# Kernel tuning notes

Hardware: AMD Instinct MI355X
Metric: run time of the kernel (lower is better)

Reference implementation:

```python
import jax, jax.numpy as jnp
import numpy as np

B, T, D_MODEL, HEAD_DIM = 4, 4096, 1024, 2


def setup_inputs() -> dict:
    key = jax.random.key(0)
    kx, kq, kk, kv = jax.random.split(key, 4)
    x = jax.random.normal(kx, (B, T, D_MODEL), dtype=jnp.float32)
    # nn.Linear weights: (out_features, in_features), applied as x @ W.T
    s_qk = 1.0 / np.sqrt(D_MODEL)
    W_Q = jax.random.uniform(kq, (HEAD_DIM, D_MODEL), minval=-s_qk, maxval=s_qk, dtype=jnp.float32)
    W_K = jax.random.uniform(kk, (HEAD_DIM, D_MODEL), minval=-s_qk, maxval=s_qk, dtype=jnp.float32)
    W_V = jax.random.uniform(kv, (D_MODEL, D_MODEL), minval=-s_qk, maxval=s_qk, dtype=jnp.float32)
    # strict upper-triangular True = masked (future positions)
    causal_mask = jnp.triu(jnp.ones((T, T), dtype=bool), k=1)[None, :, :]
    return {"x": x, "W_Q": W_Q, "W_K": W_K, "W_V": W_V, "causal_mask": causal_mask}


def reference(x, W_Q, W_K, W_V, causal_mask):
    # x: (B, T, d_model)
    Q = jnp.einsum('btd,hd->bth', x, W_Q)   # (B, T, head_dim)
    K = jnp.einsum('bsd,hd->bsh', x, W_K)   # (B, S, head_dim)
    V = jnp.einsum('bsd,ed->bse', x, W_V)   # (B, S, d_model)
    scores = jnp.einsum('bth,bsh->bts', Q, K)              # (B, T, S)
    scores = jnp.where(causal_mask, -jnp.inf, scores)
    max_idx = jnp.argmax(scores, axis=-1)                  # (B, T)
    # one-hot scatter + bmm in the original == hard gather of V rows
    out = jnp.take_along_axis(V, max_idx[..., None], axis=1)  # (B, T, d_model)
    return out
```

## Files before the change

### kernel.cpp

```cpp
#include <hip/hip_runtime.h>
#include <math.h>

#define TT 4096
#define DM 1024
#define BB 4
#define BT (BB * TT)
#define SENTINEL 0x7fffffff


__device__ __forceinline__ float dot4(const float4 a, const float4 b) {
    return a.x * b.x + a.y * b.y + a.z * b.z + a.w * b.w;
}

__global__ __launch_bounds__(256) void qk_kernel(const float* __restrict__ x,
                                                 const float* __restrict__ wq,
                                                 const float* __restrict__ wk,
                                                 float* __restrict__ Q,
                                                 float* __restrict__ K,
                                                 int* __restrict__ rep,
                                                 int* __restrict__ cnt) {
    __shared__ float4 wqs0[256], wqs1[256], wks0[256], wks1[256];
    const int tid = threadIdx.x;
    const int row0 = blockIdx.x * 4;

    wqs0[tid] = ((const float4*)(wq))[tid];
    wqs1[tid] = ((const float4*)(wq + DM))[tid];
    wks0[tid] = ((const float4*)(wk))[tid];
    wks1[tid] = ((const float4*)(wk + DM))[tid];

    if (tid < 4) rep[row0 + tid] = SENTINEL;
    if (blockIdx.x == 0 && tid == 4) cnt[0] = 0;
    __syncthreads();

    const int wave = tid >> 6, lane = tid & 63;
    const int row = row0 + wave;
    const float4* xr = (const float4*)(x + (size_t)row * DM);

    float s0 = 0.f, s1 = 0.f, s2 = 0.f, s3 = 0.f;
    #pragma unroll
    for (int j = 0; j < 4; ++j) {
        const float4 xv = xr[j * 64 + lane];
        s0 += dot4(xv, wqs0[j * 64 + lane]);
        s1 += dot4(xv, wqs1[j * 64 + lane]);
        s2 += dot4(xv, wks0[j * 64 + lane]);
        s3 += dot4(xv, wks1[j * 64 + lane]);
    }
    #pragma unroll
    for (int off = 32; off > 0; off >>= 1) {
        s0 += __shfl_down(s0, off);
        s1 += __shfl_down(s1, off);
        s2 += __shfl_down(s2, off);
        s3 += __shfl_down(s3, off);
    }
    if (lane == 0) {
        ((float2*)Q)[row] = make_float2(s0, s1);
        ((float2*)K)[row] = make_float2(s2, s3);
    }
}

__global__ __launch_bounds__(256) void argmax_kernel(const float* __restrict__ Q,
                                                     const float* __restrict__ K,
                                                     int* __restrict__ idx,
                                                     int* __restrict__ rep,
                                                     int* __restrict__ list,
                                                     int* __restrict__ cnt) {
    __shared__ float2 ks[TT];
    const int b  = blockIdx.x >> 10;
    const int tg = blockIdx.x & 1023;
    const int tid = threadIdx.x;
    const int nfill = tg * 4 + 4;

    const float2* kb = (const float2*)(K + (size_t)b * TT * 2);
    for (int i = tid; i < nfill; i += 256) ks[i] = kb[i];
    __syncthreads();

    const int wave = tid >> 6, lane = tid & 63;
    const int t = tg * 4 + wave;
    const float2 q = ((const float2*)Q)[b * TT + t];

    float best = -INFINITY;
    int bi = 0x7fffffff;
    int s = lane;
    while (s + 192 <= t) {
        const float2 k0 = ks[s];
        const float2 k1 = ks[s + 64];
        const float2 k2 = ks[s + 128];
        const float2 k3 = ks[s + 192];
        const float c0 = q.x * k0.x + q.y * k0.y;
        const float c1 = q.x * k1.x + q.y * k1.y;
        const float c2 = q.x * k2.x + q.y * k2.y;
        const float c3 = q.x * k3.x + q.y * k3.y;
        if (c0 > best) { best = c0; bi = s; }
        if (c1 > best) { best = c1; bi = s + 64; }
        if (c2 > best) { best = c2; bi = s + 128; }
        if (c3 > best) { best = c3; bi = s + 192; }
        s += 256;
    }
    while (s <= t) {
        const float2 kv = ks[s];
        const float sc = q.x * kv.x + q.y * kv.y;
        if (sc > best) { best = sc; bi = s; }
        s += 64;
    }
    #pragma unroll
    for (int off = 32; off > 0; off >>= 1) {
        const float ov = __shfl_down(best, off);
        const int   oi = __shfl_down(bi, off);
        if (ov > best || (ov == best && oi < bi)) { best = ov; bi = oi; }
    }
    if (lane == 0) {
        idx[b * TT + t] = bi;
        const int old = atomicMin(&rep[b * TT + bi], t);
        if (old == SENTINEL) {
            const int p = atomicAdd(cnt, 1);
            list[p] = b * TT + bi;
        }
    }
}

__global__ __launch_bounds__(256) void vrow_kernel(const float* __restrict__ x,
                                                   const float* __restrict__ wv,
                                                   const int* __restrict__ rep,
                                                   const int* __restrict__ list,
                                                   const int* __restrict__ cnt,
                                                   float* __restrict__ out) {
    const int tid = threadIdx.x, wave = tid >> 6, lane = tid & 63;
    const int slice = blockIdx.x >> 3;
    const int usub  = blockIdx.x & 7;
    const int e = slice * 4 + wave;

    const float4* wrow = (const float4*)(wv + (size_t)e * DM);
    const float4 w0 = wrow[lane];
    const float4 w1 = wrow[lane + 64];
    const float4 w2 = wrow[lane + 128];
    const float4 w3 = wrow[lane + 192];

    const int n = cnt[0];
    for (int li = usub; li < n; li += 8) {
        const int bs = list[li];
        const int b  = bs >> 12;
        const int r  = rep[bs];
        const float4* xr = (const float4*)(x + (size_t)bs * DM);
        const float4 x0 = xr[lane];
        const float4 x1 = xr[lane + 64];
        const float4 x2 = xr[lane + 128];
        const float4 x3 = xr[lane + 192];

        float sum = dot4(w0, x0) + dot4(w1, x1) + dot4(w2, x2) + dot4(w3, x3);
        #pragma unroll
        for (int off = 32; off > 0; off >>= 1) sum += __shfl_down(sum, off);
        if (lane == 0) out[((size_t)(b * TT + r)) * DM + e] = sum;
    }
}

__global__ __launch_bounds__(256) void gather_kernel(const int* __restrict__ idx,
                                                     const int* __restrict__ rep,
                                                     float* __restrict__ out) {
    const int bt = blockIdx.x;
    const int b = bt >> 12, t = bt & (TT - 1);
    const int s = idx[bt];
    const int r = rep[b * TT + s];
    if (r == t) return;
    const float4* src = (const float4*)(out + ((size_t)(b * TT + r)) * DM);
    float4* dst = (float4*)(out + (size_t)bt * DM);
    dst[threadIdx.x] = src[threadIdx.x];
}

extern "C" void kernel_launch(void* const* d_in, const int* in_sizes, int n_in,
                              void* d_out, int out_size, void* d_ws, size_t ws_size,
                              hipStream_t stream) {
    const float* x  = (const float*)d_in[0];
    const float* wq = (const float*)d_in[1];
    const float* wk = (const float*)d_in[2];
    const float* wv = (const float*)d_in[3];
    float* out = (float*)d_out;

    char* ws = (char*)d_ws;
    float* Q    = (float*)(ws);
    float* K    = (float*)(ws + 131072);
    int*   idx  = (int*)  (ws + 262144);
    int*   rep  = (int*)  (ws + 327680);
    int*   list = (int*)  (ws + 393216);
    int*   cnt  = (int*)  (ws + 458752);

    qk_kernel<<<BT / 4, 256, 0, stream>>>(x, wq, wk, Q, K, rep, cnt);
    argmax_kernel<<<4096, 256, 0, stream>>>(Q, K, idx, rep, list, cnt);
    vrow_kernel<<<2048, 256, 0, stream>>>(x, wv, rep, list, cnt, out);
    gather_kernel<<<BT, 256, 0, stream>>>(idx, rep, out);
}
```

Baseline: 228.5 us.

## Vectorize argmax key loads and compute four V outputs per wave

The argmax scan now reads two keys per float4 LDS load and handles four keys per iteration with fewer load instructions. The V-row kernel gives each wave four W_V rows held in registers, so each loaded x row feeds four dot products. It writes the four results as one float4 and launches half as many blocks with a 16-way stride over the unique-row list. This trades more registers per thread and fewer blocks for less redundant x traffic and fewer shuffle reductions per output.

```diff
diff --git a/kernel.cpp b/kernel.cpp
--- a/kernel.cpp
+++ b/kernel.cpp
@@ -77,30 +77,33 @@
     const int wave = tid >> 6, lane = tid & 63;
     const int t = tg * 4 + wave;
     const float2 q = ((const float2*)Q)[b * TT + t];
+    const float4* kp = (const float4*)ks;
 
     float best = -INFINITY;
     int bi = 0x7fffffff;
-    int s = lane;
-    while (s + 192 <= t) {
-        const float2 k0 = ks[s];
-        const float2 k1 = ks[s + 64];
-        const float2 k2 = ks[s + 128];
-        const float2 k3 = ks[s + 192];
-        const float c0 = q.x * k0.x + q.y * k0.y;
-        const float c1 = q.x * k1.x + q.y * k1.y;
-        const float c2 = q.x * k2.x + q.y * k2.y;
-        const float c3 = q.x * k3.x + q.y * k3.y;
-        if (c0 > best) { best = c0; bi = s; }
-        if (c1 > best) { best = c1; bi = s + 64; }
-        if (c2 > best) { best = c2; bi = s + 128; }
-        if (c3 > best) { best = c3; bi = s + 192; }
-        s += 256;
-    }
-    while (s <= t) {
-        const float2 kv = ks[s];
-        const float sc = q.x * kv.x + q.y * kv.y;
-        if (sc > best) { best = sc; bi = s; }
-        s += 64;
+    int p = lane;
+    while (2 * (p + 64) + 1 <= t) {
+        const float4 a = kp[p];
+        const float4 c = kp[p + 64];
+        const float c0 = q.x * a.x + q.y * a.y;
+        const float c1 = q.x * a.z + q.y * a.w;
+        const float c2 = q.x * c.x + q.y * c.y;
+        const float c3 = q.x * c.z + q.y * c.w;
+        if (c0 > best) { best = c0; bi = 2 * p; }
+        if (c1 > best) { best = c1; bi = 2 * p + 1; }
+        if (c2 > best) { best = c2; bi = 2 * (p + 64); }
+        if (c3 > best) { best = c3; bi = 2 * (p + 64) + 1; }
+        p += 128;
+    }
+    while (2 * p <= t) {
+        const float4 a = kp[p];
+        const float c0 = q.x * a.x + q.y * a.y;
+        if (c0 > best) { best = c0; bi = 2 * p; }
+        if (2 * p + 1 <= t) {
+            const float c1 = q.x * a.z + q.y * a.w;
+            if (c1 > best) { best = c1; bi = 2 * p + 1; }
+        }
+        p += 64;
     }
     #pragma unroll
     for (int off = 32; off > 0; off >>= 1) {
@@ -112,8 +115,8 @@
         idx[b * TT + t] = bi;
         const int old = atomicMin(&rep[b * TT + bi], t);
         if (old == SENTINEL) {
-            const int p = atomicAdd(cnt, 1);
-            list[p] = b * TT + bi;
+            const int pp = atomicAdd(cnt, 1);
+            list[pp] = b * TT + bi;
         }
     }
 }
@@ -125,31 +128,45 @@
                                                    const int* __restrict__ cnt,
                                                    float* __restrict__ out) {
     const int tid = threadIdx.x, wave = tid >> 6, lane = tid & 63;
-    const int slice = blockIdx.x >> 3;
-    const int usub  = blockIdx.x & 7;
-    const int e = slice * 4 + wave;
-
-    const float4* wrow = (const float4*)(wv + (size_t)e * DM);
-    const float4 w0 = wrow[lane];
-    const float4 w1 = wrow[lane + 64];
-    const float4 w2 = wrow[lane + 128];
-    const float4 w3 = wrow[lane + 192];
+    const int slice = blockIdx.x >> 4;
+    const int usub  = blockIdx.x & 15;
+    const int e0 = slice * 16 + wave * 4;
+
+    float4 w[4][4];
+    #pragma unroll
+    for (int r = 0; r < 4; ++r) {
+        const float4* wr = (const float4*)(wv + (size_t)(e0 + r) * DM);
+        #pragma unroll
+        for (int j = 0; j < 4; ++j) w[r][j] = wr[j * 64 + lane];
+    }
 
     const int n = cnt[0];
-    for (int li = usub; li < n; li += 8) {
+    for (int li = usub; li < n; li += 16) {
         const int bs = list[li];
         const int b  = bs >> 12;
         const int r  = rep[bs];
         const float4* xr = (const float4*)(x + (size_t)bs * DM);
-        const float4 x0 = xr[lane];
-        const float4 x1 = xr[lane + 64];
-        const float4 x2 = xr[lane + 128];
-        const float4 x3 = xr[lane + 192];
-
-        float sum = dot4(w0, x0) + dot4(w1, x1) + dot4(w2, x2) + dot4(w3, x3);
-        #pragma unroll
-        for (int off = 32; off > 0; off >>= 1) sum += __shfl_down(sum, off);
-        if (lane == 0) out[((size_t)(b * TT + r)) * DM + e] = sum;
+        float4 xv[4];
+        #pragma unroll
+        for (int j = 0; j < 4; ++j) xv[j] = xr[j * 64 + lane];
+
+        float s0 = 0.f, s1 = 0.f, s2 = 0.f, s3 = 0.f;
+        #pragma unroll
+        for (int j = 0; j < 4; ++j) {
+            s0 += dot4(w[0][j], xv[j]);
+            s1 += dot4(w[1][j], xv[j]);
+            s2 += dot4(w[2][j], xv[j]);
+            s3 += dot4(w[3][j], xv[j]);
+        }
+        #pragma unroll
+        for (int off = 32; off > 0; off >>= 1) {
+            s0 += __shfl_down(s0, off);
+            s1 += __shfl_down(s1, off);
+            s2 += __shfl_down(s2, off);
+            s3 += __shfl_down(s3, off);
+        }
+        if (lane == 0)
+            *(float4*)(out + ((size_t)(b * TT + r)) * DM + e0) = make_float4(s0, s1, s2, s3);
     }
 }
 
@@ -185,6 +202,6 @@
 
     qk_kernel<<<BT / 4, 256, 0, stream>>>(x, wq, wk, Q, K, rep, cnt);
     argmax_kernel<<<4096, 256, 0, stream>>>(Q, K, idx, rep, list, cnt);
-    vrow_kernel<<<2048, 256, 0, stream>>>(x, wv, rep, list, cnt, out);
+    vrow_kernel<<<1024, 256, 0, stream>>>(x, wv, rep, list, cnt, out);
     gather_kernel<<<BT, 256, 0, stream>>>(idx, rep, out);
 }
```

After: 215.5 us. 5.7% less time.
